# Kernel optimization log

Hardware: AMD Instinct MI355X
Metric: run time of the kernel (lower is better)

The kernel has to match this reference:

```python
import jax, jax.numpy as jnp
import numpy as np

N = 8192      # num nodes
E = 262144    # num edges (avg degree 32)
IN = 512
HID = 512
LAT = 128


def setup_inputs() -> dict:
    key = jax.random.key(0)
    ks = jax.random.split(key, 8)
    edge_index = jax.random.randint(ks[0], (2, E), 0, N, dtype=jnp.int64 if jax.config.read('jax_enable_x64') else jnp.int32)
    x = jax.random.normal(ks[1], (N, IN), jnp.float32)
    def w(k, i, o):
        return jax.random.normal(k, (i, o), jnp.float32) * (1.0 / np.sqrt(i))
    return {
        'edge_index': edge_index,
        'x': x,
        'W1': w(ks[2], IN, HID), 'b1': jnp.zeros((HID,), jnp.float32),
        'Wmu': w(ks[3], HID, LAT), 'bmu': jnp.zeros((LAT,), jnp.float32),
        'Wlv': w(ks[4], HID, LAT), 'blv': jnp.zeros((LAT,), jnp.float32),
    }


def gcn_conv(x, row, col, W, b):
    # PyG GCNConv: h = x W; symmetric norm with self-loops (added by caller);
    # out[i] = sum_{(j->i)} d_j^{-1/2} d_i^{-1/2} h[j] + b
    h = x @ W
    ones = jnp.ones((row.shape[0],), h.dtype)
    deg = jax.ops.segment_sum(ones, col, num_segments=N)  # in-degree incl. self-loop
    dinv_sqrt = jnp.where(deg > 0, jax.lax.rsqrt(jnp.maximum(deg, 1e-12)), 0.0)
    norm = dinv_sqrt[row] * dinv_sqrt[col]                # [E+N]
    out = jax.ops.segment_sum(norm[:, None] * h[row], col, num_segments=N)
    return out + b


def reference(edge_index, x, W1, b1, Wmu, bmu, Wlv, blv):
    # add self-loops once, reuse for all layers
    loops = jnp.arange(N, dtype=edge_index.dtype)
    row = jnp.concatenate([edge_index[0], loops])
    col = jnp.concatenate([edge_index[1], loops])

    h = jax.nn.relu(gcn_conv(x, row, col, W1, b1))
    mu = gcn_conv(h, row, col, Wmu, bmu)
    logvar = gcn_conv(h, row, col, Wlv, blv)
    z = mu  # eval-mode reparameterize (deterministic)
    A_pred = jax.nn.sigmoid(z @ z.T)  # [N, N] dot-product decode
    return (A_pred, mu, logvar, z)
```

## Files before the change

### kernel.cpp

```cpp
#include <hip/hip_runtime.h>

#define NNODES 8192
#define NEDGES 262144
#define FIN 512
#define FHID 512
#define FLAT 128

typedef unsigned short bfu;
typedef __attribute__((ext_vector_type(8))) short short8;
typedef __attribute__((ext_vector_type(4))) float f32x4;
typedef __attribute__((ext_vector_type(2))) float f32x2;
typedef __attribute__((ext_vector_type(4))) unsigned short us4;

__device__ __forceinline__ float bf2f(unsigned short u) {
    union { unsigned int i; float f; } c; c.i = ((unsigned int)u) << 16; return c.f;
}
__device__ __forceinline__ unsigned short f2bf(float f) {
    union { float f; unsigned int i; } c; c.f = f;
    unsigned int i = c.i;
    unsigned int r = (i + 0x7FFFu + ((i >> 16) & 1u)) >> 16;
    return (unsigned short)r;
}

__global__ void k_zero(int* p, int n) {
    int i = blockIdx.x * blockDim.x + threadIdx.x;
    if (i < n) p[i] = 0;
}

__global__ void k_count(const int* __restrict__ ei, int* __restrict__ deg) {
    int e = blockIdx.x * blockDim.x + threadIdx.x;
    if (e < NEDGES) atomicAdd(&deg[ei[NEDGES + e]], 1);
}

__global__ void k_scan(const int* __restrict__ deg, int* __restrict__ row_start,
                       float* __restrict__ dinv) {
    __shared__ int part[256];
    int t = threadIdx.x, base = t * 32;
    int s = 0;
    for (int i = 0; i < 32; i++) s += deg[base + i];
    part[t] = s;
    __syncthreads();
    for (int off = 1; off < 256; off <<= 1) {
        int v = (t >= off) ? part[t - off] : 0;
        __syncthreads();
        part[t] += v;
        __syncthreads();
    }
    int run = (t == 0) ? 0 : part[t - 1];
    for (int i = 0; i < 32; i++) {
        int d = deg[base + i];
        row_start[base + i] = run;
        run += d;
        dinv[base + i] = rsqrtf((float)(d + 1));
    }
    if (t == 255) row_start[NNODES] = run;
}

__global__ void k_scatter(const int* __restrict__ ei, const int* __restrict__ row_start,
                          int* __restrict__ cursor, int* __restrict__ csr,
                          const float* __restrict__ dinv, float* __restrict__ wcsr) {
    int e = blockIdx.x * blockDim.x + threadIdx.x;
    if (e < NEDGES) {
        int src = ei[e];
        int dst = ei[NEDGES + e];
        int p = atomicAdd(&cursor[dst], 1);
        int pos = row_start[dst] + p;
        csr[pos] = src;
        wcsr[pos] = dinv[src];
    }
}

__global__ void k_cvt_x(const float* __restrict__ x, bfu* __restrict__ xb) {
    int i = blockIdx.x * blockDim.x + threadIdx.x;
    const float4 v = ((const float4*)x)[i];
    ushort2 lo = {f2bf(v.x), f2bf(v.y)};
    ushort2 hi = {f2bf(v.z), f2bf(v.w)};
    ((ushort2*)xb)[2 * i] = lo;
    ((ushort2*)xb)[2 * i + 1] = hi;
}

__global__ void k_bt1_t(const float* __restrict__ W, bfu* __restrict__ Bt) {
    __shared__ bfu tile[32][33];
    int tx = threadIdx.x & 31, ty = threadIdx.x >> 5;
    int nb = blockIdx.x & 15, kb = blockIdx.x >> 4;
    int n0 = nb * 32, k0 = kb * 32;
#pragma unroll
    for (int i = 0; i < 32; i += 8)
        tile[ty + i][tx] = f2bf(W[(size_t)(k0 + ty + i) * 512 + n0 + tx]);
    __syncthreads();
#pragma unroll
    for (int i = 0; i < 32; i += 8)
        Bt[(size_t)(n0 + ty + i) * 512 + k0 + tx] = tile[tx][ty + i];
}

__global__ void k_bt2_t(const float* __restrict__ Wmu, const float* __restrict__ Wlv,
                        bfu* __restrict__ Bt) {
    __shared__ bfu tile[32][33];
    int tx = threadIdx.x & 31, ty = threadIdx.x >> 5;
    int nb = blockIdx.x & 7, kb = blockIdx.x >> 3;
    int n0 = nb * 32, k0 = kb * 32;
    const float* Wsel = (n0 < 128) ? Wmu : Wlv;
    int noff = (n0 < 128) ? 0 : 128;
#pragma unroll
    for (int i = 0; i < 32; i += 8)
        tile[ty + i][tx] = f2bf(Wsel[(size_t)(k0 + ty + i) * 128 + (n0 + tx - noff)]);
    __syncthreads();
#pragma unroll
    for (int i = 0; i < 32; i += 8)
        Bt[(size_t)(n0 + ty + i) * 512 + k0 + tx] = tile[tx][ty + i];
}

template <int ACT, int TM, int TN, typename CT>
__global__ void k_gemm_nt(const bfu* __restrict__ A, const bfu* __restrict__ Bt,
                          CT* __restrict__ C, int M, int N, int K) {
    int wid  = (blockIdx.x * blockDim.x + threadIdx.x) >> 6;
    int lane = threadIdx.x & 63;
    int l = lane & 15, q = lane >> 4;
    int tn = N / (16 * TN);
    int m0 = (wid / tn) * (16 * TM), n0 = (wid % tn) * (16 * TN);

    f32x4 acc[TM][TN];
#pragma unroll
    for (int a = 0; a < TM; a++)
#pragma unroll
        for (int b = 0; b < TN; b++) acc[a][b] = (f32x4){0.f, 0.f, 0.f, 0.f};

    const bfu* Ap = A + (size_t)(m0 + l) * K + q * 8;
    const bfu* Bp = Bt + (size_t)(n0 + l) * K + q * 8;

    for (int k0 = 0; k0 < K; k0 += 32) {
        short8 av[TM], bv[TN];
#pragma unroll
        for (int mi = 0; mi < TM; mi++)
            av[mi] = *(const short8*)(Ap + (size_t)mi * 16 * K + k0);
#pragma unroll
        for (int ni = 0; ni < TN; ni++)
            bv[ni] = *(const short8*)(Bp + (size_t)ni * 16 * K + k0);
#pragma unroll
        for (int mi = 0; mi < TM; mi++)
#pragma unroll
            for (int ni = 0; ni < TN; ni++)
                acc[mi][ni] = __builtin_amdgcn_mfma_f32_16x16x32_bf16(bv[ni], av[mi],
                                                                     acc[mi][ni], 0, 0, 0);
    }

#pragma unroll
    for (int mi = 0; mi < TM; mi++) {
        int row = m0 + mi * 16 + l;
#pragma unroll
        for (int ni = 0; ni < TN; ni++) {
            int col = n0 + ni * 16 + q * 4;
            f32x4 v = acc[mi][ni];
            if (ACT == 2) {
#pragma unroll
                for (int r = 0; r < 4; r++)
                    v[r] = __builtin_amdgcn_rcpf(1.0f + __expf(-v[r]));
            }
            if constexpr (sizeof(CT) == 2) {
                us4 o = {f2bf(v[0]), f2bf(v[1]), f2bf(v[2]), f2bf(v[3])};
                *(us4*)(C + (size_t)row * N + col) = o;
            } else {
                __builtin_nontemporal_store(v, (f32x4*)(C + (size_t)row * N + col));
            }
        }
    }
}

template <int F>
__device__ __forceinline__ void agg_core(const bfu* __restrict__ hin,
                                         const int* __restrict__ csr,
                                         const float* __restrict__ wcsr,
                                         int s, int e, int i, int f, float di,
                                         float& a0, float& a1) {
    a0 = 0.f; a1 = 0.f;
    int ed = s;
    for (; ed + 4 <= e; ed += 4) {
        int s0 = csr[ed], s1 = csr[ed + 1], s2 = csr[ed + 2], s3 = csr[ed + 3];
        float w0 = wcsr[ed], w1 = wcsr[ed + 1], w2 = wcsr[ed + 2], w3 = wcsr[ed + 3];
        unsigned int p0 = *(const unsigned int*)(hin + (size_t)s0 * F + f);
        unsigned int p1 = *(const unsigned int*)(hin + (size_t)s1 * F + f);
        unsigned int p2 = *(const unsigned int*)(hin + (size_t)s2 * F + f);
        unsigned int p3 = *(const unsigned int*)(hin + (size_t)s3 * F + f);
        a0 += w0 * bf2f((unsigned short)(p0 & 0xFFFF));
        a1 += w0 * bf2f((unsigned short)(p0 >> 16));
        a0 += w1 * bf2f((unsigned short)(p1 & 0xFFFF));
        a1 += w1 * bf2f((unsigned short)(p1 >> 16));
        a0 += w2 * bf2f((unsigned short)(p2 & 0xFFFF));
        a1 += w2 * bf2f((unsigned short)(p2 >> 16));
        a0 += w3 * bf2f((unsigned short)(p3 & 0xFFFF));
        a1 += w3 * bf2f((unsigned short)(p3 >> 16));
    }
    for (; ed < e; ed++) {
        int src = csr[ed];
        float w = wcsr[ed];
        unsigned int pk = *(const unsigned int*)(hin + (size_t)src * F + f);
        a0 += w * bf2f((unsigned short)(pk & 0xFFFF));
        a1 += w * bf2f((unsigned short)(pk >> 16));
    }
    unsigned int pk = *(const unsigned int*)(hin + (size_t)i * F + f);
    a0 += di * bf2f((unsigned short)(pk & 0xFFFF));
    a1 += di * bf2f((unsigned short)(pk >> 16));
}

__global__ void k_agg1(const bfu* __restrict__ hin, const int* __restrict__ csr,
                       const float* __restrict__ wcsr, const int* __restrict__ rs,
                       const float* __restrict__ dinv, const float* __restrict__ bias,
                       bfu* __restrict__ hout) {
    int i = blockIdx.x;
    int f = threadIdx.x * 2;
    float di = dinv[i];
    float a0, a1;
    agg_core<FHID>(hin, csr, wcsr, rs[i], rs[i + 1], i, f, di, a0, a1);
    float o0 = fmaxf(di * a0 + bias[f], 0.f);
    float o1 = fmaxf(di * a1 + bias[f + 1], 0.f);
    unsigned int outw = (unsigned int)f2bf(o0) | ((unsigned int)f2bf(o1) << 16);
    *(unsigned int*)(hout + (size_t)i * FHID + f) = outw;
}

__global__ void k_agg2(const bfu* __restrict__ hin, const int* __restrict__ csr,
                       const float* __restrict__ wcsr, const int* __restrict__ rs,
                       const float* __restrict__ dinv, const float* __restrict__ bmu,
                       const float* __restrict__ blv, float* __restrict__ out_mu,
                       float* __restrict__ out_lv, float* __restrict__ out_z,
                       bfu* __restrict__ ws_z) {
    int i = blockIdx.x;
    int f = threadIdx.x * 2;
    float di = dinv[i];
    float a0, a1;
    agg_core<256>(hin, csr, wcsr, rs[i], rs[i + 1], i, f, di, a0, a1);
    float v0 = di * a0, v1 = di * a1;
    if (f < 128) {
        v0 += bmu[f]; v1 += bmu[f + 1];
        f32x2 fv = {v0, v1};
        __builtin_nontemporal_store(fv, (f32x2*)(out_mu + (size_t)i * FLAT + f));
        __builtin_nontemporal_store(fv, (f32x2*)(out_z + (size_t)i * FLAT + f));
        unsigned int bw = (unsigned int)f2bf(v0) | ((unsigned int)f2bf(v1) << 16);
        *(unsigned int*)(ws_z + (size_t)i * FLAT + f) = bw;
    } else {
        int fl = f - 128;
        v0 += blv[fl]; v1 += blv[fl + 1];
        f32x2 fv = {v0, v1};
        __builtin_nontemporal_store(fv, (f32x2*)(out_lv + (size_t)i * FLAT + fl));
    }
}

extern "C" void kernel_launch(void* const* d_in, const int* in_sizes, int n_in,
                              void* d_out, int out_size, void* d_ws, size_t ws_size,
                              hipStream_t stream) {
    const int*   ei  = (const int*)d_in[0];
    const float* x   = (const float*)d_in[1];
    const float* W1  = (const float*)d_in[2];
    const float* b1  = (const float*)d_in[3];
    const float* Wmu = (const float*)d_in[4];
    const float* bmu = (const float*)d_in[5];
    const float* Wlv = (const float*)d_in[6];
    const float* blv = (const float*)d_in[7];
    float* out = (float*)d_out;

    char* wsb = (char*)d_ws;
    size_t off = 0;
    auto alloc = [&](size_t bytes) -> char* {
        char* p = wsb + off;
        off += (bytes + 255) & ~(size_t)255;
        return p;
    };
    int*   deg       = (int*)alloc(NNODES * 4);
    int*   cursor    = (int*)alloc(NNODES * 4);
    int*   row_start = (int*)alloc((NNODES + 1) * 4);
    float* dinv      = (float*)alloc(NNODES * 4);
    int*   csr       = (int*)alloc(NEDGES * 4);
    float* wcsr      = (float*)alloc(NEDGES * 4);
    bfu*   Bt1       = (bfu*)alloc(512 * 512 * 2);
    bfu*   Bt2       = (bfu*)alloc(256 * 512 * 2);
    bfu*   xb        = (bfu*)alloc((size_t)NNODES * FIN * 2);
    bfu*   h0        = (bfu*)alloc((size_t)NNODES * FHID * 2);
    bfu*   h         = (bfu*)alloc((size_t)NNODES * FHID * 2);
    bfu*   hml       = (bfu*)alloc((size_t)NNODES * 256 * 2);
    bfu*   zb        = (bfu*)alloc((size_t)NNODES * FLAT * 2);

    float* out_mu = out + (size_t)NNODES * NNODES;
    float* out_lv = out_mu + (size_t)NNODES * FLAT;
    float* out_z  = out_lv + (size_t)NNODES * FLAT;

    k_zero<<<(2 * NNODES + 255) / 256, 256, 0, stream>>>(deg, 2 * NNODES);
    k_count<<<NEDGES / 256, 256, 0, stream>>>(ei, deg);
    k_scan<<<1, 256, 0, stream>>>(deg, row_start, dinv);
    k_scatter<<<NEDGES / 256, 256, 0, stream>>>(ei, row_start, cursor, csr, dinv, wcsr);
    k_bt1_t<<<256, 256, 0, stream>>>(W1, Bt1);
    k_bt2_t<<<128, 256, 0, stream>>>(Wmu, Wlv, Bt2);
    k_cvt_x<<<(NNODES * FIN / 4) / 256, 256, 0, stream>>>(x, xb);

    k_gemm_nt<0, 4, 2, bfu><<<(8192 / 64) * (512 / 32) / 4, 256, 0, stream>>>(
        xb, Bt1, h0, 8192, 512, 512);
    k_agg1<<<NNODES, 256, 0, stream>>>(h0, csr, wcsr, row_start, dinv, b1, h);

    k_gemm_nt<0, 2, 2, bfu><<<(8192 / 32) * (256 / 32) / 4, 256, 0, stream>>>(
        h, Bt2, hml, 8192, 256, 512);
    k_agg2<<<NNODES, 128, 0, stream>>>(hml, csr, wcsr, row_start, dinv, bmu, blv,
                                       out_mu, out_lv, out_z, zb);

    k_gemm_nt<2, 4, 4, float><<<(8192 / 64) * (8192 / 64) / 4, 256, 0, stream>>>(
        zb, zb, out, 8192, 8192, 128);
}
```

Measured before the change: 486.5 us.

## Exploit symmetry of z z^T decode and merge weight/input prep kernels

Replaces the full N×N decode GEMM with a kernel that computes only the upper-triangular 64×64 tiles. Each off-diagonal tile is written both directly and, after a transpose through LDS, to its mirrored position. This roughly halves the MFMA and sigmoid work, but the 268 MB fp32 output write stays the same and the transposed stores are narrower per lane. The three preprocessing kernels are also fused into one launch to cut launch overhead.

```diff
diff --git a/kernel.cpp b/kernel.cpp
--- a/kernel.cpp
+++ b/kernel.cpp
@@ -1,4 +1,5 @@
 #include <hip/hip_runtime.h>
+#include <math.h>
 
 #define NNODES 8192
 #define NEDGES 262144
@@ -70,49 +71,50 @@
     }
 }
 
-__global__ void k_cvt_x(const float* __restrict__ x, bfu* __restrict__ xb) {
-    int i = blockIdx.x * blockDim.x + threadIdx.x;
-    const float4 v = ((const float4*)x)[i];
-    ushort2 lo = {f2bf(v.x), f2bf(v.y)};
-    ushort2 hi = {f2bf(v.z), f2bf(v.w)};
-    ((ushort2*)xb)[2 * i] = lo;
-    ((ushort2*)xb)[2 * i + 1] = hi;
-}
-
-__global__ void k_bt1_t(const float* __restrict__ W, bfu* __restrict__ Bt) {
+__global__ void k_prep_const(const float* __restrict__ W1, const float* __restrict__ Wmu,
+                             const float* __restrict__ Wlv, const float* __restrict__ x,
+                             bfu* __restrict__ Bt1, bfu* __restrict__ Bt2,
+                             bfu* __restrict__ xb) {
     __shared__ bfu tile[32][33];
-    int tx = threadIdx.x & 31, ty = threadIdx.x >> 5;
-    int nb = blockIdx.x & 15, kb = blockIdx.x >> 4;
-    int n0 = nb * 32, k0 = kb * 32;
-#pragma unroll
-    for (int i = 0; i < 32; i += 8)
-        tile[ty + i][tx] = f2bf(W[(size_t)(k0 + ty + i) * 512 + n0 + tx]);
-    __syncthreads();
-#pragma unroll
-    for (int i = 0; i < 32; i += 8)
-        Bt[(size_t)(n0 + ty + i) * 512 + k0 + tx] = tile[tx][ty + i];
-}
-
-__global__ void k_bt2_t(const float* __restrict__ Wmu, const float* __restrict__ Wlv,
-                        bfu* __restrict__ Bt) {
-    __shared__ bfu tile[32][33];
-    int tx = threadIdx.x & 31, ty = threadIdx.x >> 5;
-    int nb = blockIdx.x & 7, kb = blockIdx.x >> 3;
-    int n0 = nb * 32, k0 = kb * 32;
-    const float* Wsel = (n0 < 128) ? Wmu : Wlv;
-    int noff = (n0 < 128) ? 0 : 128;
-#pragma unroll
-    for (int i = 0; i < 32; i += 8)
-        tile[ty + i][tx] = f2bf(Wsel[(size_t)(k0 + ty + i) * 128 + (n0 + tx - noff)]);
-    __syncthreads();
-#pragma unroll
-    for (int i = 0; i < 32; i += 8)
-        Bt[(size_t)(n0 + ty + i) * 512 + k0 + tx] = tile[tx][ty + i];
-}
-
-template <int ACT, int TM, int TN, typename CT>
+    int b = blockIdx.x;
+    if (b < 256) {
+        int tx = threadIdx.x & 31, ty = threadIdx.x >> 5;
+        int nb = b & 15, kb = b >> 4;
+        int n0 = nb * 32, k0 = kb * 32;
+#pragma unroll
+        for (int i = 0; i < 32; i += 8)
+            tile[ty + i][tx] = f2bf(W1[(size_t)(k0 + ty + i) * 512 + n0 + tx]);
+        __syncthreads();
+#pragma unroll
+        for (int i = 0; i < 32; i += 8)
+            Bt1[(size_t)(n0 + ty + i) * 512 + k0 + tx] = tile[tx][ty + i];
+    } else if (b < 384) {
+        int bb = b - 256;
+        int tx = threadIdx.x & 31, ty = threadIdx.x >> 5;
+        int nb = bb & 7, kb = bb >> 3;
+        int n0 = nb * 32, k0 = kb * 32;
+        const float* Wsel = (n0 < 128) ? Wmu : Wlv;
+        int noff = (n0 < 128) ? 0 : 128;
+#pragma unroll
+        for (int i = 0; i < 32; i += 8)
+            tile[ty + i][tx] = f2bf(Wsel[(size_t)(k0 + ty + i) * 128 + (n0 + tx - noff)]);
+        __syncthreads();
+#pragma unroll
+        for (int i = 0; i < 32; i += 8)
+            Bt2[(size_t)(n0 + ty + i) * 512 + k0 + tx] = tile[tx][ty + i];
+    } else {
+        int i = (b - 384) * 256 + threadIdx.x;
+        const float4 v = ((const float4*)x)[i];
+        ushort2 lo = {f2bf(v.x), f2bf(v.y)};
+        ushort2 hi = {f2bf(v.z), f2bf(v.w)};
+        ((ushort2*)xb)[2 * i] = lo;
+        ((ushort2*)xb)[2 * i + 1] = hi;
+    }
+}
+
+template <int TM, int TN>
 __global__ void k_gemm_nt(const bfu* __restrict__ A, const bfu* __restrict__ Bt,
-                          CT* __restrict__ C, int M, int N, int K) {
+                          bfu* __restrict__ C, int M, int N, int K) {
     int wid  = (blockIdx.x * blockDim.x + threadIdx.x) >> 6;
     int lane = threadIdx.x & 63;
     int l = lane & 15, q = lane >> 4;
@@ -151,16 +153,88 @@
         for (int ni = 0; ni < TN; ni++) {
             int col = n0 + ni * 16 + q * 4;
             f32x4 v = acc[mi][ni];
-            if (ACT == 2) {
+            us4 o = {f2bf(v[0]), f2bf(v[1]), f2bf(v[2]), f2bf(v[3])};
+            *(us4*)(C + (size_t)row * N + col) = o;
+        }
+    }
+}
+
+__global__ __launch_bounds__(256) void k_decode_sym(const bfu* __restrict__ Z,
+                                                    float* __restrict__ C) {
+    __shared__ float ldsT[4][2][16][68];
+    int wid  = (blockIdx.x * blockDim.x + threadIdx.x) >> 6;
+    int wv   = threadIdx.x >> 6;
+    int lane = threadIdx.x & 63;
+    int l = lane & 15, q = lane >> 4;
+
+    int idx = wid;
+    int ti = (int)((257.0 - sqrt(66049.0 - 8.0 * (double)idx)) * 0.5);
+    if (ti > 127) ti = 127;
+    if (ti < 0) ti = 0;
+    while (ti > 0 && (ti * (257 - ti)) / 2 > idx) ti--;
+    while (ti < 127 && ((ti + 1) * (256 - ti)) / 2 <= idx) ti++;
+    int tj = ti + (idx - (ti * (257 - ti)) / 2);
+    int m0 = ti * 64, n0 = tj * 64;
+
+    f32x4 acc[4][4];
+#pragma unroll
+    for (int a = 0; a < 4; a++)
+#pragma unroll
+        for (int b = 0; b < 4; b++) acc[a][b] = (f32x4){0.f, 0.f, 0.f, 0.f};
+
+    const bfu* Ap = Z + (size_t)(m0 + l) * 128 + q * 8;
+    const bfu* Bp = Z + (size_t)(n0 + l) * 128 + q * 8;
+
+#pragma unroll
+    for (int k0 = 0; k0 < 128; k0 += 32) {
+        short8 av[4], bv[4];
+#pragma unroll
+        for (int mi = 0; mi < 4; mi++)
+            av[mi] = *(const short8*)(Ap + (size_t)mi * 16 * 128 + k0);
+#pragma unroll
+        for (int ni = 0; ni < 4; ni++)
+            bv[ni] = *(const short8*)(Bp + (size_t)ni * 16 * 128 + k0);
+#pragma unroll
+        for (int mi = 0; mi < 4; mi++)
+#pragma unroll
+            for (int ni = 0; ni < 4; ni++)
+                acc[mi][ni] = __builtin_amdgcn_mfma_f32_16x16x32_bf16(bv[ni], av[mi],
+                                                                     acc[mi][ni], 0, 0, 0);
+    }
+
+#pragma unroll
+    for (int mi = 0; mi < 4; mi++)
+#pragma unroll
+        for (int ni = 0; ni < 4; ni++)
+#pragma unroll
+            for (int r = 0; r < 4; r++)
+                acc[mi][ni][r] = __builtin_amdgcn_rcpf(1.0f + __expf(-acc[mi][ni][r]));
+
+#pragma unroll
+    for (int mi = 0; mi < 4; mi++) {
+        int row = m0 + mi * 16 + l;
+#pragma unroll
+        for (int ni = 0; ni < 4; ni++) {
+            int col = n0 + ni * 16 + q * 4;
+            __builtin_nontemporal_store(acc[mi][ni], (f32x4*)(C + (size_t)row * 8192 + col));
+        }
+    }
+
+    if (ti != tj) {
+#pragma unroll
+        for (int ni = 0; ni < 4; ni++) {
+            int p = ni & 1;
+#pragma unroll
+            for (int mi = 0; mi < 4; mi++)
 #pragma unroll
                 for (int r = 0; r < 4; r++)
-                    v[r] = __builtin_amdgcn_rcpf(1.0f + __expf(-v[r]));
-            }
-            if constexpr (sizeof(CT) == 2) {
-                us4 o = {f2bf(v[0]), f2bf(v[1]), f2bf(v[2]), f2bf(v[3])};
-                *(us4*)(C + (size_t)row * N + col) = o;
-            } else {
-                __builtin_nontemporal_store(v, (f32x4*)(C + (size_t)row * N + col));
+                    ldsT[wv][p][q * 4 + r][mi * 16 + l] = acc[mi][ni][r];
+            asm volatile("s_waitcnt lgkmcnt(0)" ::: "memory");
+#pragma unroll
+            for (int j = 0; j < 16; j++) {
+                float v = ldsT[wv][p][j][lane];
+                __builtin_nontemporal_store(
+                    v, C + (size_t)(n0 + ni * 16 + j) * 8192 + m0 + lane);
             }
         }
     }
@@ -286,19 +360,16 @@
     k_count<<<NEDGES / 256, 256, 0, stream>>>(ei, deg);
     k_scan<<<1, 256, 0, stream>>>(deg, row_start, dinv);
     k_scatter<<<NEDGES / 256, 256, 0, stream>>>(ei, row_start, cursor, csr, dinv, wcsr);
-    k_bt1_t<<<256, 256, 0, stream>>>(W1, Bt1);
-    k_bt2_t<<<128, 256, 0, stream>>>(Wmu, Wlv, Bt2);
-    k_cvt_x<<<(NNODES * FIN / 4) / 256, 256, 0, stream>>>(x, xb);
-
-    k_gemm_nt<0, 4, 2, bfu><<<(8192 / 64) * (512 / 32) / 4, 256, 0, stream>>>(
+    k_prep_const<<<256 + 128 + 4096, 256, 0, stream>>>(W1, Wmu, Wlv, x, Bt1, Bt2, xb);
+
+    k_gemm_nt<4, 2><<<(8192 / 64) * (512 / 32) / 4, 256, 0, stream>>>(
         xb, Bt1, h0, 8192, 512, 512);
     k_agg1<<<NNODES, 256, 0, stream>>>(h0, csr, wcsr, row_start, dinv, b1, h);
 
-    k_gemm_nt<0, 2, 2, bfu><<<(8192 / 32) * (256 / 32) / 4, 256, 0, stream>>>(
+    k_gemm_nt<2, 2><<<(8192 / 32) * (256 / 32) / 4, 256, 0, stream>>>(
         h, Bt2, hml, 8192, 256, 512);
     k_agg2<<<NNODES, 128, 0, stream>>>(hml, csr, wcsr, row_start, dinv, bmu, blv,
                                        out_mu, out_lv, out_z, zb);
 
-    k_gemm_nt<2, 4, 4, float><<<(8192 / 64) * (8192 / 64) / 4, 256, 0, stream>>>(
-        zb, zb, out, 8192, 8192, 128);
-}
+    k_decode_sym<<<8256 / 4, 256, 0, stream>>>(zb, out);
+}
```

Result: faster. 450.9 us (-7.3%).
